# Optimization experiments

Hardware: AMD Instinct MI355X
Metric: run time of the kernel (lower is better)

The kernel has to match this reference:

```python
import jax, jax.numpy as jnp
import numpy as np

D_K = 64

def setup_inputs() -> dict:
    key = jax.random.key(0)
    kx, kq, kk, kv = jax.random.split(key, 4)
    B, T, D = 4, 2048, 1024
    s = 1.0 / np.sqrt(D)
    return {
        "x": jax.random.normal(kx, (B, T, D), dtype=jnp.float32),
        "Wq": jax.random.normal(kq, (D, D_K), dtype=jnp.float32) * s,
        "Wk": jax.random.normal(kk, (D, D_K), dtype=jnp.float32) * s,
        "Wv": jax.random.normal(kv, (D, D_K), dtype=jnp.float32) * s,
    }

def reference(x, Wq, Wk, Wv):
    # x: [B, T, D]; Wq/Wk/Wv: [D, d_k]
    Q = x @ Wq  # [B, T, d_k]
    K = x @ Wk
    V = x @ Wv
    scale = 1.0 / jnp.sqrt(jnp.asarray(Q.shape[-1], Q.dtype))
    scores = jnp.einsum('btd,bsd->bts', Q, K) * scale  # [B, T, T]
    T = scores.shape[-1]
    causal = jnp.tril(jnp.ones((T, T), dtype=bool))  # keep lower-tri incl diag
    masked = jnp.where(causal, scores, -jnp.inf)
    attn = jax.nn.softmax(masked, axis=-1)  # dropout p=0.0 -> identity
    context = jnp.einsum('bts,bsd->btd', attn, V)  # [B, T, d_k]
    return context
```

## Files before the change

### kernel.cpp

```cpp
#include <hip/hip_runtime.h>
#include <math.h>

#define BT    8192
#define TSEQ  2048
#define DIN   1024
#define DK    64

typedef __attribute__((ext_vector_type(8))) short bf16x8;
typedef __attribute__((ext_vector_type(4))) short bf16x4;
typedef __attribute__((ext_vector_type(4))) float f32x4;

static __device__ inline unsigned short f2bf(float f) {
    union { float f; unsigned u; } v; v.f = f;
    unsigned r = v.u + 0x7fff + ((v.u >> 16) & 1);
    return (unsigned short)(r >> 16);
}

static __device__ inline bf16x4 cvt4(float4 a) {
    bf16x4 r;
    r[0] = (short)f2bf(a.x); r[1] = (short)f2bf(a.y);
    r[2] = (short)f2bf(a.z); r[3] = (short)f2bf(a.w);
    return r;
}

__global__ __launch_bounds__(256) void wt_kernel(
    const float* __restrict__ Wq, const float* __restrict__ Wk,
    const float* __restrict__ Wv, unsigned short* __restrict__ WT)
{
    __shared__ float ws[64][65];
    const int tid = threadIdx.x;
    const int mat = blockIdx.x >> 4;
    const int k0  = (blockIdx.x & 15) << 6;
    const float* W = (mat == 0) ? Wq : ((mat == 1) ? Wk : Wv);

    const int j = tid & 63;
    for (int i = tid >> 6; i < 64; i += 4)
        ws[i][j] = W[(size_t)(k0 + i) * DK + j];
    __syncthreads();

    const int n  = tid & 63;
    const int c0 = (tid >> 6) << 4;
    unsigned short* dst = WT + (size_t)(mat * 64 + n) * DIN + k0 + c0;
    #pragma unroll
    for (int c = 0; c < 16; ++c) dst[c] = f2bf(ws[c0 + c][n]);
}

__global__ __launch_bounds__(256, 2) void proj_kernel(
    const float* __restrict__ x, const unsigned short* __restrict__ WT,
    unsigned short* __restrict__ Qb, unsigned short* __restrict__ Kb,
    unsigned short* __restrict__ VT)
{
    __shared__ unsigned short xs[16][1032];
    __shared__ unsigned short wtb[192][72];
    const int tid = threadIdx.x;
    const int m0 = blockIdx.x * 16;

    {
        const int r = tid >> 4;
        const int c = (tid & 15) << 2;
        const float* src = x + (size_t)(m0 + r) * DIN + c;
        float4 tmp[16];
        #pragma unroll
        for (int s = 0; s < 16; ++s) tmp[s] = *(const float4*)(src + s * 64);
        #pragma unroll
        for (int s = 0; s < 16; ++s) *(bf16x4*)&xs[r][c + s * 64] = cvt4(tmp[s]);
    }

    const int lane = tid & 63;
    const int w    = tid >> 6;
    const int lr = lane & 15, lg = lane >> 4;

    f32x4 acc[3];
    #pragma unroll
    for (int nt = 0; nt < 3; ++nt) acc[nt] = (f32x4){0.f, 0.f, 0.f, 0.f};

    const unsigned short* wt_w = WT + (size_t)w * 48 * DIN;
    bf16x8 cur[6], nxt[6];
    #pragma unroll
    for (int i = 0; i < 6; ++i) {
        const int c = lane + i * 64;
        const int nl = c >> 3;
        const int sl = c & 7;
        cur[i] = *(const bf16x8*)(wt_w + (size_t)nl * DIN + (sl << 3));
    }

    __syncthreads();

    for (int kc = 0; kc < 16; ++kc) {
        const int k0 = kc << 6;

        if (kc + 1 < 16) {
            #pragma unroll
            for (int i = 0; i < 6; ++i) {
                const int c = lane + i * 64;
                const int nl = c >> 3;
                const int sl = c & 7;
                nxt[i] = *(const bf16x8*)(wt_w + (size_t)nl * DIN
                                          + (k0 + 64) + (sl << 3));
            }
        }

        #pragma unroll
        for (int i = 0; i < 6; ++i) {
            const int c = lane + i * 64;
            const int n = w * 48 + (c >> 3);
            const int sl = c & 7;
            *(bf16x8*)&wtb[n][((sl + n) & 7) << 3] = cur[i];
        }
        asm volatile("s_waitcnt lgkmcnt(0)" ::: "memory");

        #pragma unroll
        for (int st = 0; st < 2; ++st) {
            const bf16x8 af = *(const bf16x8*)&xs[lr][k0 + (st << 5) + (lg << 3)];
            #pragma unroll
            for (int nt = 0; nt < 3; ++nt) {
                const int n = w * 48 + nt * 16 + lr;
                const int sl = (st << 2) + lg;
                const bf16x8 bf = *(const bf16x8*)&wtb[n][((sl + n) & 7) << 3];
                acc[nt] = __builtin_amdgcn_mfma_f32_16x16x32_bf16(af, bf, acc[nt], 0, 0, 0);
            }
        }

        if (kc + 1 < 16) {
            #pragma unroll
            for (int i = 0; i < 6; ++i) cur[i] = nxt[i];
        }
    }

    const float qsc = 0.125f * 1.44269504088896340736f;
    #pragma unroll
    for (int nt = 0; nt < 3; ++nt) {
        const int gct = w * 3 + nt;
        if (gct < 8) {
            #pragma unroll
            for (int r = 0; r < 4; ++r) {
                const int row = m0 + (lg << 2) + r;
                const float vv = acc[nt][r];
                if (gct < 4) Qb[(size_t)row * DK + gct * 16 + lr] = f2bf(vv * qsc);
                else         Kb[(size_t)row * DK + (gct - 4) * 16 + lr] = f2bf(vv);
            }
        } else {
            const int d = (gct - 8) * 16 + lr;
            const int t = m0 + (lg << 2);
            const int tb = t & (TSEQ - 1);
            const size_t tile = (size_t)(t >> 11) * 32 + (tb >> 6);
            ushort4 pk;
            pk.x = f2bf(acc[nt][0]); pk.y = f2bf(acc[nt][1]);
            pk.z = f2bf(acc[nt][2]); pk.w = f2bf(acc[nt][3]);
            *(ushort4*)&VT[(tile * DK + d) * 64 + (tb & 63)] = pk;
        }
    }
}

__global__ __launch_bounds__(256, 2) void attn_kernel(
    const unsigned short* __restrict__ Qb, const unsigned short* __restrict__ Kb,
    const unsigned short* __restrict__ VT, float* __restrict__ O)
{
    __shared__ __align__(16) unsigned short P_lds[4][16][72];
    __shared__ float Opart[4][16][68];
    __shared__ float mpart[4][16];
    __shared__ float Lpart[4][16];

    const int lane = threadIdx.x & 63;
    const int w    = threadIdx.x >> 6;
    const int i    = blockIdx.x;
    const int half = i >> 8;
    const int k    = i & 255;
    const int batch = k & 3;
    const int j    = k >> 2;
    const int qt_local = half ? j : (127 - j);
    const int q0 = (batch << 11) + (qt_local << 4);
    const int t0 = qt_local << 4;
    const int b  = batch;
    const int lr = lane & 15;
    const int lg = lane >> 4;

    const unsigned short* Qrow = Qb + (size_t)(q0 + lr) * DK + (lg << 3);
    const bf16x8 qf0 = *(const bf16x8*)(Qrow);
    const bf16x8 qf1 = *(const bf16x8*)(Qrow + 32);

    const unsigned short* Kbase = Kb + (size_t)b * TSEQ * DK;
    const unsigned short* Vbase = VT + (size_t)b * 32 * DK * 64;

    f32x4 oacc[4];
    #pragma unroll
    for (int dt = 0; dt < 4; ++dt) oacc[dt] = (f32x4){0.f, 0.f, 0.f, 0.f};
    float m[4] = {-INFINITY, -INFINITY, -INFINITY, -INFINITY};
    float L[4] = {0.f, 0.f, 0.f, 0.f};

    const int nkb = (t0 >> 6) + 1;

    for (int kb = w; kb < nkb; kb += 4) {
        const int s0 = kb << 6;

        bf16x8 kf0[4], kf1[4];
        #pragma unroll
        for (int ct = 0; ct < 4; ++ct) {
            const unsigned short* Krow =
                Kbase + (size_t)(s0 + ct * 16 + lr) * DK + (lg << 3);
            kf0[ct] = *(const bf16x8*)(Krow);
            kf1[ct] = *(const bf16x8*)(Krow + 32);
        }

        bf16x8 vf0[4], vf1[4];
        {
            const unsigned short* Vtile = Vbase + (size_t)kb * DK * 64;
            #pragma unroll
            for (int dt = 0; dt < 4; ++dt) {
                const unsigned short* Vrow = Vtile + (dt * 16 + lr) * 64 + (lg << 3);
                vf0[dt] = *(const bf16x8*)(Vrow);
                vf1[dt] = *(const bf16x8*)(Vrow + 32);
            }
        }

        f32x4 s[4];
        #pragma unroll
        for (int ct = 0; ct < 4; ++ct) {
            f32x4 a = (f32x4){0.f, 0.f, 0.f, 0.f};
            a = __builtin_amdgcn_mfma_f32_16x16x32_bf16(qf0, kf0[ct], a, 0, 0, 0);
            a = __builtin_amdgcn_mfma_f32_16x16x32_bf16(qf1, kf1[ct], a, 0, 0, 0);
            s[ct] = a;
        }

        if (kb == nkb - 1) {
            #pragma unroll
            for (int ct = 0; ct < 4; ++ct)
                #pragma unroll
                for (int r = 0; r < 4; ++r)
                    if (s0 + ct * 16 + lr > t0 + lg * 4 + r) s[ct][r] = -INFINITY;
        }

        float pm[4];
        #pragma unroll
        for (int r = 0; r < 4; ++r)
            pm[r] = fmaxf(fmaxf(s[0][r], s[1][r]), fmaxf(s[2][r], s[3][r]));

        bool near = true;
        #pragma unroll
        for (int r = 0; r < 4; ++r)
            near = near && (pm[r] - m[r] <= 8.0f);

        if (!__all(near)) {
            float tmax[4];
            #pragma unroll
            for (int r = 0; r < 4; ++r) tmax[r] = pm[r];
            #pragma unroll
            for (int off = 1; off < 16; off <<= 1)
                #pragma unroll
                for (int r = 0; r < 4; ++r)
                    tmax[r] = fmaxf(tmax[r], __shfl_xor(tmax[r], off));

            float f[4];
            #pragma unroll
            for (int r = 0; r < 4; ++r) {
                const float mn = fmaxf(m[r], tmax[r]);
                f[r] = exp2f(m[r] - mn);
                m[r] = mn;
            }
            #pragma unroll
            for (int r = 0; r < 4; ++r) L[r] *= f[r];
            #pragma unroll
            for (int r = 0; r < 4; ++r) {
                oacc[0][r] *= f[r]; oacc[1][r] *= f[r];
                oacc[2][r] *= f[r]; oacc[3][r] *= f[r];
            }
        }

        float ps[4] = {0.f, 0.f, 0.f, 0.f};
        unsigned short pb[4][4];
        #pragma unroll
        for (int ct = 0; ct < 4; ++ct)
            #pragma unroll
            for (int r = 0; r < 4; ++r) {
                const float p = exp2f(s[ct][r] - m[r]);
                ps[r] += p;
                pb[ct][r] = f2bf(p);
            }
        #pragma unroll
        for (int r = 0; r < 4; ++r) L[r] += ps[r];

        #pragma unroll
        for (int ct = 0; ct < 4; ++ct)
            #pragma unroll
            for (int r = 0; r < 4; ++r)
                P_lds[w][lg * 4 + r][ct * 16 + lr] = pb[ct][r];
        asm volatile("s_waitcnt lgkmcnt(0)" ::: "memory");
        const bf16x8 pf0 = *(const bf16x8*)&P_lds[w][lr][(lg << 3)];
        const bf16x8 pf1 = *(const bf16x8*)&P_lds[w][lr][32 + (lg << 3)];

        #pragma unroll
        for (int dt = 0; dt < 4; ++dt) {
            oacc[dt] = __builtin_amdgcn_mfma_f32_16x16x32_bf16(pf0, vf0[dt], oacc[dt], 0, 0, 0);
            oacc[dt] = __builtin_amdgcn_mfma_f32_16x16x32_bf16(pf1, vf1[dt], oacc[dt], 0, 0, 0);
        }
    }

    #pragma unroll
    for (int off = 1; off < 16; off <<= 1)
        #pragma unroll
        for (int r = 0; r < 4; ++r) L[r] += __shfl_xor(L[r], off);

    #pragma unroll
    for (int dt = 0; dt < 4; ++dt)
        #pragma unroll
        for (int r = 0; r < 4; ++r)
            Opart[w][(lg << 2) + r][dt * 16 + lr] = oacc[dt][r];
    if (lr == 0) {
        #pragma unroll
        for (int r = 0; r < 4; ++r) {
            mpart[w][(lg << 2) + r] = m[r];
            Lpart[w][(lg << 2) + r] = L[r];
        }
    }
    __syncthreads();

    #pragma unroll
    for (int r = 0; r < 4; ++r) {
        const int row = (lg << 2) + r;
        const float M = fmaxf(fmaxf(mpart[0][row], mpart[1][row]),
                              fmaxf(mpart[2][row], mpart[3][row]));
        float Lf = 0.f, o = 0.f;
        #pragma unroll
        for (int v = 0; v < 4; ++v) {
            const float fv = exp2f(mpart[v][row] - M);
            Lf += fv * Lpart[v][row];
            o  += fv * Opart[v][row][(w << 4) + lr];
        }
        O[(size_t)(q0 + row) * DK + (w << 4) + lr] = o / Lf;
    }
}

extern "C" void kernel_launch(void* const* d_in, const int* in_sizes, int n_in,
                              void* d_out, int out_size, void* d_ws, size_t ws_size,
                              hipStream_t stream) {
    const float* x  = (const float*)d_in[0];
    const float* Wq = (const float*)d_in[1];
    const float* Wk = (const float*)d_in[2];
    const float* Wv = (const float*)d_in[3];
    float* O = (float*)d_out;

    unsigned short* Qb = (unsigned short*)d_ws;
    unsigned short* Kb = Qb + (size_t)BT * DK;
    unsigned short* VT = Kb + (size_t)BT * DK;
    unsigned short* WT = VT + (size_t)BT * DK;

    wt_kernel  <<<dim3(48),  dim3(256), 0, stream>>>(Wq, Wk, Wv, WT);
    proj_kernel<<<dim3(512), dim3(256), 0, stream>>>(x, WT, Qb, Kb, VT);
    attn_kernel<<<dim3(512), dim3(256), 0, stream>>>(Qb, Kb, VT, O);
}
```

Baseline: 42.05 us.

## Block weight layout per k-chunk and read MFMA B operands directly from global

The transposed bf16 weights are now stored in k-chunk-blocked order (16 chunks of 192x64), so each wave can load its MFMA B fragments straight from global/L2. This removes the per-iteration LDS staging of weights, the register double buffer, and the LDS wait. It trades LDS traffic and LDS footprint for repeated global loads, which may hit L2 well because all blocks share the small weight matrix.

```diff
diff --git a/kernel.cpp b/kernel.cpp
--- a/kernel.cpp
+++ b/kernel.cpp
@@ -25,12 +25,13 @@
 
 __global__ __launch_bounds__(256) void wt_kernel(
     const float* __restrict__ Wq, const float* __restrict__ Wk,
-    const float* __restrict__ Wv, unsigned short* __restrict__ WT)
+    const float* __restrict__ Wv, unsigned short* __restrict__ WTB)
 {
     __shared__ float ws[64][65];
     const int tid = threadIdx.x;
     const int mat = blockIdx.x >> 4;
-    const int k0  = (blockIdx.x & 15) << 6;
+    const int kc  = blockIdx.x & 15;
+    const int k0  = kc << 6;
     const float* W = (mat == 0) ? Wq : ((mat == 1) ? Wk : Wv);
 
     const int j = tid & 63;
@@ -40,18 +41,17 @@
 
     const int n  = tid & 63;
     const int c0 = (tid >> 6) << 4;
-    unsigned short* dst = WT + (size_t)(mat * 64 + n) * DIN + k0 + c0;
+    unsigned short* dst = WTB + ((size_t)kc * 192 + mat * 64 + n) * 64 + c0;
     #pragma unroll
     for (int c = 0; c < 16; ++c) dst[c] = f2bf(ws[c0 + c][n]);
 }
 
 __global__ __launch_bounds__(256, 2) void proj_kernel(
-    const float* __restrict__ x, const unsigned short* __restrict__ WT,
+    const float* __restrict__ x, const unsigned short* __restrict__ WTB,
     unsigned short* __restrict__ Qb, unsigned short* __restrict__ Kb,
     unsigned short* __restrict__ VT)
 {
     __shared__ unsigned short xs[16][1032];
-    __shared__ unsigned short wtb[192][72];
     const int tid = threadIdx.x;
     const int m0 = blockIdx.x * 16;
 
@@ -74,56 +74,21 @@
     #pragma unroll
     for (int nt = 0; nt < 3; ++nt) acc[nt] = (f32x4){0.f, 0.f, 0.f, 0.f};
 
-    const unsigned short* wt_w = WT + (size_t)w * 48 * DIN;
-    bf16x8 cur[6], nxt[6];
-    #pragma unroll
-    for (int i = 0; i < 6; ++i) {
-        const int c = lane + i * 64;
-        const int nl = c >> 3;
-        const int sl = c & 7;
-        cur[i] = *(const bf16x8*)(wt_w + (size_t)nl * DIN + (sl << 3));
-    }
+    const unsigned short* wrow = WTB + ((size_t)w * 48 + lr) * 64 + (lg << 3);
 
     __syncthreads();
 
+    #pragma unroll 4
     for (int kc = 0; kc < 16; ++kc) {
-        const int k0 = kc << 6;
-
-        if (kc + 1 < 16) {
-            #pragma unroll
-            for (int i = 0; i < 6; ++i) {
-                const int c = lane + i * 64;
-                const int nl = c >> 3;
-                const int sl = c & 7;
-                nxt[i] = *(const bf16x8*)(wt_w + (size_t)nl * DIN
-                                          + (k0 + 64) + (sl << 3));
-            }
-        }
-
-        #pragma unroll
-        for (int i = 0; i < 6; ++i) {
-            const int c = lane + i * 64;
-            const int n = w * 48 + (c >> 3);
-            const int sl = c & 7;
-            *(bf16x8*)&wtb[n][((sl + n) & 7) << 3] = cur[i];
-        }
-        asm volatile("s_waitcnt lgkmcnt(0)" ::: "memory");
-
         #pragma unroll
         for (int st = 0; st < 2; ++st) {
-            const bf16x8 af = *(const bf16x8*)&xs[lr][k0 + (st << 5) + (lg << 3)];
+            const bf16x8 af = *(const bf16x8*)&xs[lr][(kc << 6) + (st << 5) + (lg << 3)];
             #pragma unroll
             for (int nt = 0; nt < 3; ++nt) {
-                const int n = w * 48 + nt * 16 + lr;
-                const int sl = (st << 2) + lg;
-                const bf16x8 bf = *(const bf16x8*)&wtb[n][((sl + n) & 7) << 3];
+                const bf16x8 bf = *(const bf16x8*)(wrow + (size_t)kc * 12288
+                                                   + nt * 1024 + (st << 5));
                 acc[nt] = __builtin_amdgcn_mfma_f32_16x16x32_bf16(af, bf, acc[nt], 0, 0, 0);
             }
-        }
-
-        if (kc + 1 < 16) {
-            #pragma unroll
-            for (int i = 0; i < 6; ++i) cur[i] = nxt[i];
         }
     }
 
@@ -339,12 +304,12 @@
     const float* Wv = (const float*)d_in[3];
     float* O = (float*)d_out;
 
-    unsigned short* Qb = (unsigned short*)d_ws;
-    unsigned short* Kb = Qb + (size_t)BT * DK;
-    unsigned short* VT = Kb + (size_t)BT * DK;
-    unsigned short* WT = VT + (size_t)BT * DK;
-
-    wt_kernel  <<<dim3(48),  dim3(256), 0, stream>>>(Wq, Wk, Wv, WT);
-    proj_kernel<<<dim3(512), dim3(256), 0, stream>>>(x, WT, Qb, Kb, VT);
+    unsigned short* Qb  = (unsigned short*)d_ws;
+    unsigned short* Kb  = Qb + (size_t)BT * DK;
+    unsigned short* VT  = Kb + (size_t)BT * DK;
+    unsigned short* WTB = VT + (size_t)BT * DK;
+
+    wt_kernel  <<<dim3(48),  dim3(256), 0, stream>>>(Wq, Wk, Wv, WTB);
+    proj_kernel<<<dim3(512), dim3(256), 0, stream>>>(x, WTB, Qb, Kb, VT);
     attn_kernel<<<dim3(512), dim3(256), 0, stream>>>(Qb, Kb, VT, O);
 }
```

Result: slower. 55.31 us (+31.5%).
